# Performance work log

Hardware: AMD Instinct MI355X
Metric: run time of the kernel (lower is better)

The kernel has to match this reference:

```python
import jax, jax.numpy as jnp
import numpy as np
import math

B, N, L = 1, 256, 384
DM, DP, H, D = 256, 128, 8, 32  # d_msa, d_pair, n_head, d_hidden


def ln(x, g, b):
    m = x.mean(-1, keepdims=True)
    v = ((x - m) ** 2).mean(-1, keepdims=True)
    return (x - m) * jax.lax.rsqrt(v + 1e-5) * g + b


def setup_inputs() -> dict:
    key = jax.random.key(0)
    ks = jax.random.split(key, 12)
    s = 0.02
    return dict(
        msa=jax.random.normal(ks[0], (B, N, L, DM), jnp.float32),
        pair=jax.random.normal(ks[1], (B, L, L, DP), jnp.float32),
        ln_msa_g=jnp.ones((DM,), jnp.float32),
        ln_msa_b=jnp.zeros((DM,), jnp.float32),
        ln_pair_g=jnp.ones((DP,), jnp.float32),
        ln_pair_b=jnp.zeros((DP,), jnp.float32),
        sw_wq=s * jax.random.normal(ks[2], (DM, H * D), jnp.float32),
        sw_bq=jnp.zeros((H * D,), jnp.float32),
        sw_wk=s * jax.random.normal(ks[3], (DM, H * D), jnp.float32),
        sw_bk=jnp.zeros((H * D,), jnp.float32),
        wq=s * jax.random.normal(ks[4], (DM, H * D), jnp.float32),
        wk=s * jax.random.normal(ks[5], (DM, H * D), jnp.float32),
        wv=s * jax.random.normal(ks[6], (DM, H * D), jnp.float32),
        wb=s * jax.random.normal(ks[7], (DP, H), jnp.float32),
        wg=s * jax.random.normal(ks[8], (DM, H * D), jnp.float32),
        bg=jnp.ones((H * D,), jnp.float32),
        wo=s * jax.random.normal(ks[9], (H * D, DM), jnp.float32),
        bo=jnp.zeros((DM,), jnp.float32),
    )


def reference(msa, pair, ln_msa_g, ln_msa_b, ln_pair_g, ln_pair_b,
              sw_wq, sw_bq, sw_wk, sw_bk, wq, wk, wv, wb, wg, bg, wo, bo):
    m = ln(msa, ln_msa_g, ln_msa_b)  # (B,N,L,DM) -- LayerNorm(msa)
    inv_sqrt_d = 1.0 / math.sqrt(D)

    # --- SequenceWeight: attention of target seq (row 0) over all MSA rows ---
    qsw = ((m[:, 0] @ sw_wq) + sw_bq).reshape(B, 1, L, H, D) * inv_sqrt_d
    ksw = ((m @ sw_wk) + sw_bk).reshape(B, N, L, H, D)
    sw_logits = jnp.einsum('bqihd,bnihd->bnihq', qsw, ksw)  # (B,N,L,H,1)
    seq_weight = jax.nn.softmax(sw_logits, axis=1)  # softmax over MSA depth N; dropout is eval no-op

    # --- row attention with pair bias ---
    q = (m @ wq).reshape(B, N, L, H, D) * seq_weight  # query scaled by per-row seq weight
    k = (m @ wk).reshape(B, N, L, H, D) * inv_sqrt_d
    attn = jnp.einsum('bnihd,bnjhd->bijh', q, k)  # sum over MSA rows n -> (B,L,L,H)
    attn = attn + ln(pair, ln_pair_g, ln_pair_b) @ wb  # additive pair bias
    attn = jax.nn.softmax(attn, axis=-2)  # softmax over j (dim=-2)

    v = (m @ wv).reshape(B, N, L, H, D)
    out = jnp.einsum('bijh,bnjhd->bnihd', attn, v).reshape(B, N, L, H * D)
    gate = jax.nn.sigmoid((m @ wg) + bg)
    out = out * gate
    return out @ wo + bo  # (B,N,L,DM)
```

## Files before the change

### kernel.cpp

```cpp
#include <hip/hip_runtime.h>
#include <math.h>

typedef unsigned short u16;
typedef __bf16 bf16x8 __attribute__((ext_vector_type(8)));
typedef float f32x4 __attribute__((ext_vector_type(4)));

#define DEV static __device__ __forceinline__

DEV float b2f(u16 u) { union { unsigned int i; float f; } v; v.i = ((unsigned int)u) << 16; return v.f; }
DEV u16 f2b(float f) {
  union { float f; unsigned int i; } v; v.f = f;
  unsigned int x = v.i;
  unsigned int r = (x + 0x7fffu + ((x >> 16) & 1u)) >> 16;
  return (u16)r;
}
DEV bf16x8 load8bf(const u16* p) {
  union { uint4 u; bf16x8 b; } t;
  t.u = *(const uint4*)p;
  return t.b;
}
DEV float wave_sum(float x) {
  for (int m = 32; m >= 1; m >>= 1) x += __shfl_xor(x, m, 64);
  return x;
}
DEV float wave_max(float x) {
  for (int m = 32; m >= 1; m >>= 1) x = fmaxf(x, __shfl_xor(x, m, 64));
  return x;
}

__global__ __launch_bounds__(256) void detect_dtype(const u16* __restrict__ probe, int* __restrict__ flag) {
  __shared__ float red[4];
  int wave = threadIdx.x >> 6, lane = threadIdx.x & 63;
  float v = fabsf(b2f(probe[threadIdx.x]));
  v = wave_max(v);
  if (lane == 0) red[wave] = v;
  __syncthreads();
  if (threadIdx.x == 0) {
    float m = fmaxf(fmaxf(red[0], red[1]), fmaxf(red[2], red[3]));
    *flag = (m > 1e10f) ? 1 : 0;
  }
}

struct SmallCvt {
  const void* src[9];
  int n[9];
  int off[9];
};
__global__ __launch_bounds__(256) void cvt_small(SmallCvt s, u16* __restrict__ dst, const int* __restrict__ flagp) {
  int isf32 = *flagp;
  int a = blockIdx.x;
  const void* sp = s.src[a];
  for (int i = threadIdx.x; i < s.n[a]; i += 256) {
    float v = isf32 ? ((const float*)sp)[i] : b2f(((const u16*)sp)[i]);
    dst[s.off[a] + i] = f2b(v);
  }
}

__global__ __launch_bounds__(256) void ln_msa_k(const void* __restrict__ xv, const u16* __restrict__ g,
                                                const u16* __restrict__ b, u16* __restrict__ out,
                                                const int* __restrict__ flagp) {
  int isf32 = *flagp;
  int wave = threadIdx.x >> 6, lane = threadIdx.x & 63;
  size_t row = (size_t)blockIdx.x * 4 + wave;
  float f0, f1, f2, f3;
  if (isf32) {
    float4 v = *(const float4*)((const float*)xv + row * 256 + lane * 4);
    f0 = v.x; f1 = v.y; f2 = v.z; f3 = v.w;
  } else {
    ushort4 v = *(const ushort4*)((const u16*)xv + row * 256 + lane * 4);
    f0 = b2f(v.x); f1 = b2f(v.y); f2 = b2f(v.z); f3 = b2f(v.w);
  }
  float s = wave_sum(f0 + f1 + f2 + f3);
  float s2 = wave_sum(f0 * f0 + f1 * f1 + f2 * f2 + f3 * f3);
  float mean = s * (1.f / 256.f);
  float inv = rsqrtf(s2 * (1.f / 256.f) - mean * mean + 1e-5f);
  int c0 = lane * 4;
  ushort4 gv = *(const ushort4*)(g + c0);
  ushort4 bv = *(const ushort4*)(b + c0);
  ushort4 o;
  o.x = f2b((f0 - mean) * inv * b2f(gv.x) + b2f(bv.x));
  o.y = f2b((f1 - mean) * inv * b2f(gv.y) + b2f(bv.y));
  o.z = f2b((f2 - mean) * inv * b2f(gv.z) + b2f(bv.z));
  o.w = f2b((f3 - mean) * inv * b2f(gv.w) + b2f(bv.w));
  *(ushort4*)(out + row * 256 + c0) = o;
}

struct TransArgs {
  const void* src[7];
  u16* dst[7];
};
__global__ __launch_bounds__(256) void transpose_w(TransArgs t, const int* __restrict__ flagp) {
  __shared__ float tile[32][33];
  int isf32 = *flagp;
  int m = blockIdx.z;
  const void* s = t.src[m];
  u16* d = t.dst[m];
  int bx = blockIdx.x * 32, by = blockIdx.y * 32;
  int c = threadIdx.x & 31, r0 = threadIdx.x >> 5;
  for (int rr = r0; rr < 32; rr += 8) {
    int idx = (by + rr) * 256 + bx + c;
    tile[rr][c] = isf32 ? ((const float*)s)[idx] : b2f(((const u16*)s)[idx]);
  }
  __syncthreads();
  for (int rr = r0; rr < 32; rr += 8) d[(bx + rr) * 256 + by + c] = f2b(tile[c][rr]);
}

__global__ __launch_bounds__(256) void gemmA(const u16* __restrict__ A, size_t aoff,
                                             const u16* __restrict__ WT, const u16* __restrict__ bias,
                                             void* __restrict__ outv, size_t ooff, int mode, float alpha,
                                             const float* __restrict__ sw, int n0sw,
                                             const int* __restrict__ flagp, int out_flag) {
  int isf32 = *flagp;
  int i0 = blockIdx.x * 128, n0 = blockIdx.y * 128;
  int wave = threadIdx.x >> 6, lane = threadIdx.x & 63;
  int wr = wave >> 1, wc = wave & 1;
  int l15 = lane & 15, quad = lane >> 4;
  const f32x4 fz = {0.f, 0.f, 0.f, 0.f};
  f32x4 acc[4][4];
  for (int mi = 0; mi < 4; ++mi)
    for (int ni = 0; ni < 4; ++ni) acc[mi][ni] = fz;
  int arow = i0 + wr * 64 + l15;
  int brow = n0 + wc * 64 + l15;
  const u16* ap = A + (aoff + (size_t)arow) * 256 + quad * 8;
  const u16* bp = WT + (size_t)brow * 256 + quad * 8;
  for (int k0 = 0; k0 < 256; k0 += 32) {
    bf16x8 a[4], b[4];
#pragma unroll
    for (int mi = 0; mi < 4; ++mi) a[mi] = load8bf(ap + mi * 16 * 256 + k0);
#pragma unroll
    for (int ni = 0; ni < 4; ++ni) b[ni] = load8bf(bp + ni * 16 * 256 + k0);
#pragma unroll
    for (int mi = 0; mi < 4; ++mi)
#pragma unroll
      for (int ni = 0; ni < 4; ++ni)
        acc[mi][ni] = __builtin_amdgcn_mfma_f32_16x16x32_bf16(a[mi], b[ni], acc[mi][ni], 0, 0, 0);
  }
  int f32out = out_flag && isf32;
  int nloc = blockIdx.x / 3;
#pragma unroll
  for (int mi = 0; mi < 4; ++mi) {
    int rbase = i0 + wr * 64 + mi * 16 + quad * 4;
#pragma unroll
    for (int ni = 0; ni < 4; ++ni) {
      int col = n0 + wc * 64 + ni * 16 + l15;
      float bv = bias ? b2f(bias[col]) : 0.f;
#pragma unroll
      for (int r = 0; r < 4; ++r) {
        float val = (acc[mi][ni][r] + bv) * alpha;
        if (mode == 2) {
          int i = rbase - nloc * 384 + r;
          int h = col >> 5;
          val *= sw[((size_t)(i * 8 + h)) * 256 + (n0sw + nloc)];
        }
        size_t idx = (ooff + (size_t)(rbase + r)) * 256 + col;
        if (mode == 1) {
          float gate = 1.f / (1.f + expf(-val));
          ((u16*)outv)[idx] = f2b(b2f(((u16*)outv)[idx]) * gate);
        } else if (f32out) {
          ((float*)outv)[idx] = val;
        } else {
          ((u16*)outv)[idx] = f2b(val);
        }
      }
    }
  }
}

__global__ __launch_bounds__(256) void sw_logits_c(const u16* __restrict__ qsw, const u16* __restrict__ kswc,
                                                   float* __restrict__ swlog, int n0) {
  int nl = blockIdx.y;
  int t = blockIdx.x * 256 + threadIdx.x;
  int i = t >> 3, h = t & 7;
  const u16* kr = kswc + ((size_t)(nl * 384 + i)) * 256 + h * 32;
  const u16* qr = qsw + (size_t)i * 256 + h * 32;
  float dot = 0.f;
#pragma unroll
  for (int d8 = 0; d8 < 4; ++d8) {
    union { uint4 u; u16 us[8]; } ku, qu;
    ku.u = *(const uint4*)(kr + d8 * 8);
    qu.u = *(const uint4*)(qr + d8 * 8);
#pragma unroll
    for (int j = 0; j < 8; ++j) dot += b2f(ku.us[j]) * b2f(qu.us[j]);
  }
  swlog[(size_t)(i * 8 + h) * 256 + n0 + nl] = dot;
}

__global__ __launch_bounds__(256) void sw_softmax(float* __restrict__ swlog) {
  __shared__ float red[4];
  float* p = swlog + (size_t)blockIdx.x * 256;
  int wave = threadIdx.x >> 6, lane = threadIdx.x & 63;
  float x = p[threadIdx.x];
  float m = wave_max(x);
  if (lane == 0) red[wave] = m;
  __syncthreads();
  float mx = fmaxf(fmaxf(red[0], red[1]), fmaxf(red[2], red[3]));
  __syncthreads();
  float e = expf(x - mx);
  float s = wave_sum(e);
  if (lane == 0) red[wave] = s;
  __syncthreads();
  float sum = red[0] + red[1] + red[2] + red[3];
  p[threadIdx.x] = e / sum;
}

__global__ __launch_bounds__(256) void pair_bias(const void* __restrict__ pairv, const u16* __restrict__ g,
                                                 const u16* __restrict__ b, const u16* __restrict__ wb,
                                                 float* __restrict__ attn, const int* __restrict__ flagp) {
  int isf32 = *flagp;
  int wave = threadIdx.x >> 6, lane = threadIdx.x & 63;
  size_t row = (size_t)blockIdx.x * 4 + wave;
  float v0, v1;
  if (isf32) {
    const float* pf = (const float*)pairv + row * 128 + lane * 2;
    v0 = pf[0]; v1 = pf[1];
  } else {
    const u16* pr = (const u16*)pairv + row * 128 + lane * 2;
    v0 = b2f(pr[0]); v1 = b2f(pr[1]);
  }
  float s = wave_sum(v0 + v1);
  float s2 = wave_sum(v0 * v0 + v1 * v1);
  float mean = s * (1.f / 128.f);
  float var = s2 * (1.f / 128.f) - mean * mean;
  float inv = rsqrtf(var + 1e-5f);
  int c0 = lane * 2;
  v0 = (v0 - mean) * inv * b2f(g[c0]) + b2f(b[c0]);
  v1 = (v1 - mean) * inv * b2f(g[c0 + 1]) + b2f(b[c0 + 1]);
  float ph[8];
  const u16* w0 = wb + c0 * 8;
#pragma unroll
  for (int h = 0; h < 8; ++h) ph[h] = v0 * b2f(w0[h]) + v1 * b2f(w0[8 + h]);
#pragma unroll
  for (int m = 32; m >= 1; m >>= 1)
#pragma unroll
    for (int h = 0; h < 8; ++h) ph[h] += __shfl_xor(ph[h], m, 64);
  if (lane == 0) {
#pragma unroll
    for (int h = 0; h < 8; ++h) attn[(size_t)h * 147456 + row] = ph[h];
  }
}

__global__ __launch_bounds__(256) void qk_accum_c(const u16* __restrict__ qc, const u16* __restrict__ kc,
                                                  float* __restrict__ attn, int nlen) {
  int h = blockIdx.y;
  int i0 = (blockIdx.x % 3) * 128, j0 = (blockIdx.x / 3) * 128;
  int nb = blockIdx.z * nlen;
  int wave = threadIdx.x >> 6, lane = threadIdx.x & 63;
  int wr = wave >> 1, wc = wave & 1;
  int l15 = lane & 15, quad = lane >> 4;
  const f32x4 fz = {0.f, 0.f, 0.f, 0.f};
  f32x4 acc[4][4];
  for (int mi = 0; mi < 4; ++mi)
    for (int ni = 0; ni < 4; ++ni) acc[mi][ni] = fz;
  int arow = i0 + wr * 64 + l15;
  int brow = j0 + wc * 64 + l15;
  for (int n = nb; n < nb + nlen; ++n) {
    size_t base = (size_t)n * 384;
    const u16* ap = qc + (base + arow) * 256 + h * 32 + quad * 8;
    const u16* bp = kc + (base + brow) * 256 + h * 32 + quad * 8;
    bf16x8 a[4], b[4];
#pragma unroll
    for (int mi = 0; mi < 4; ++mi) a[mi] = load8bf(ap + mi * 16 * 256);
#pragma unroll
    for (int ni = 0; ni < 4; ++ni) b[ni] = load8bf(bp + ni * 16 * 256);
#pragma unroll
    for (int mi = 0; mi < 4; ++mi)
#pragma unroll
      for (int ni = 0; ni < 4; ++ni)
        acc[mi][ni] = __builtin_amdgcn_mfma_f32_16x16x32_bf16(a[mi], b[ni], acc[mi][ni], 0, 0, 0);
  }
#pragma unroll
  for (int mi = 0; mi < 4; ++mi)
#pragma unroll
    for (int ni = 0; ni < 4; ++ni) {
      int i = i0 + wr * 64 + mi * 16 + quad * 4;
      int j = j0 + wc * 64 + ni * 16 + l15;
#pragma unroll
      for (int r = 0; r < 4; ++r)
        atomicAdd(&attn[(size_t)h * 147456 + (size_t)(i + r) * 384 + j], acc[mi][ni][r]);
    }
}

__global__ __launch_bounds__(384) void attn_softmax_k(const float* __restrict__ attn, u16* __restrict__ attn_bf) {
  __shared__ float red[6];
  size_t r = blockIdx.x;
  const float* p = attn + r * 384;
  int wave = threadIdx.x >> 6, lane = threadIdx.x & 63;
  float x = p[threadIdx.x];
  float m = wave_max(x);
  if (lane == 0) red[wave] = m;
  __syncthreads();
  float mx = red[0];
#pragma unroll
  for (int i = 1; i < 6; ++i) mx = fmaxf(mx, red[i]);
  __syncthreads();
  float e = expf(x - mx);
  float s = wave_sum(e);
  if (lane == 0) red[wave] = s;
  __syncthreads();
  float sum = 0.f;
#pragma unroll
  for (int i = 0; i < 6; ++i) sum += red[i];
  attn_bf[r * 384 + threadIdx.x] = f2b(e / sum);
}

__global__ __launch_bounds__(256) void transpose_v_c(const u16* __restrict__ vc, u16* __restrict__ vt) {
  __shared__ float tile[32][65];
  int nh = blockIdx.y;
  int nl = nh >> 3, h = nh & 7;
  int j0 = blockIdx.x * 64;
  int d = threadIdx.x & 31, jt = threadIdx.x >> 5;
  for (int jj = jt; jj < 64; jj += 8)
    tile[d][jj] = b2f(vc[((size_t)(nl * 384 + j0 + jj)) * 256 + h * 32 + d]);
  __syncthreads();
  int j = threadIdx.x & 63, dq = threadIdx.x >> 6;
  for (int dd = dq; dd < 32; dd += 4)
    vt[((size_t)(nh * 32 + dd)) * 384 + j0 + j] = f2b(tile[dd][j]);
}

__global__ __launch_bounds__(256) void pv_c(const u16* __restrict__ attn_bf, const u16* __restrict__ vt,
                                            u16* __restrict__ oc) {
  int i0 = blockIdx.x * 128;
  int nh = blockIdx.y;
  int nl = nh >> 3, h = nh & 7;
  int w = threadIdx.x >> 6, lane = threadIdx.x & 63;
  int l15 = lane & 15, quad = lane >> 4;
  const f32x4 fz = {0.f, 0.f, 0.f, 0.f};
  f32x4 acc[2][2];
  for (int mi = 0; mi < 2; ++mi)
    for (int ni = 0; ni < 2; ++ni) acc[mi][ni] = fz;
  for (int j0 = 0; j0 < 384; j0 += 32) {
    bf16x8 a[2], b[2];
#pragma unroll
    for (int mi = 0; mi < 2; ++mi)
      a[mi] = load8bf(attn_bf + ((size_t)(h * 384 + i0 + w * 32 + mi * 16 + l15)) * 384 + j0 + quad * 8);
#pragma unroll
    for (int ni = 0; ni < 2; ++ni)
      b[ni] = load8bf(vt + ((size_t)(nh * 32 + ni * 16 + l15)) * 384 + j0 + quad * 8);
#pragma unroll
    for (int mi = 0; mi < 2; ++mi)
#pragma unroll
      for (int ni = 0; ni < 2; ++ni)
        acc[mi][ni] = __builtin_amdgcn_mfma_f32_16x16x32_bf16(a[mi], b[ni], acc[mi][ni], 0, 0, 0);
  }
#pragma unroll
  for (int mi = 0; mi < 2; ++mi)
#pragma unroll
    for (int ni = 0; ni < 2; ++ni) {
      int ib = i0 + w * 32 + mi * 16 + quad * 4;
      int dcol = ni * 16 + l15;
#pragma unroll
      for (int r = 0; r < 4; ++r) {
        size_t idx = ((size_t)(nl * 384 + ib + r)) * 256 + h * 32 + dcol;
        oc[idx] = f2b(acc[mi][ni][r]);
      }
    }
}

extern "C" void kernel_launch(void* const* d_in, const int* in_sizes, int n_in,
                              void* d_out, int out_size, void* d_ws, size_t ws_size,
                              hipStream_t stream) {
  const void* msa = d_in[0];
  const void* pair = d_in[1];
  const void* ln_msa_g = d_in[2];
  const void* ln_msa_b = d_in[3];
  const void* ln_pair_g = d_in[4];
  const void* ln_pair_b = d_in[5];
  const void* sw_wq = d_in[6];
  const void* sw_bq = d_in[7];
  const void* sw_wk = d_in[8];
  const void* sw_bk = d_in[9];
  const void* wq = d_in[10];
  const void* wk = d_in[11];
  const void* wv = d_in[12];
  const void* wb = d_in[13];
  const void* wg = d_in[14];
  const void* bg = d_in[15];
  const void* wo = d_in[16];
  const void* bo = d_in[17];

  char* ws = (char*)d_ws;
  int* flag = (int*)ws;
  float* swlog = (float*)(ws + 256);
  float* attnf = (float*)(ws + 3145984);
  u16* wT = (u16*)(ws + 7864576);
  u16* qswb = (u16*)(ws + 8782080);
  u16* attnbf = (u16*)(ws + 8978688);
  u16* smallv = (u16*)(ws + 11337984);
  u16* mbf = (u16*)(ws + 11343616);
  const size_t SMALLS = 61675264ull;
  u16* c_lng = smallv + 0;
  u16* c_lnb = smallv + 256;
  u16* c_lpg = smallv + 512;
  u16* c_lpb = smallv + 640;
  u16* c_sbq = smallv + 768;
  u16* c_sbk = smallv + 1024;
  u16* c_bg = smallv + 1280;
  u16* c_bo = smallv + 1536;
  u16* c_wb = smallv + 1792;

  int NC = 256;
  while (NC > 8 && SMALLS + 3ull * (size_t)NC * 196608ull > ws_size) NC >>= 1;
  const size_t CBsz = (size_t)NC * 196608ull;
  u16* CB1 = (u16*)(ws + SMALLS);
  u16* CB2 = (u16*)(ws + SMALLS + CBsz);
  u16* CB3 = (u16*)(ws + SMALLS + 2 * CBsz);
  const int nchunks = 256 / NC;
  const int nlen = (NC < 64) ? NC : 64;

  const float isd = 0.17677669529663687f;

  detect_dtype<<<1, 256, 0, stream>>>((const u16*)msa, flag);

  SmallCvt sc;
  sc.src[0] = ln_msa_g;  sc.n[0] = 256;  sc.off[0] = 0;
  sc.src[1] = ln_msa_b;  sc.n[1] = 256;  sc.off[1] = 256;
  sc.src[2] = ln_pair_g; sc.n[2] = 128;  sc.off[2] = 512;
  sc.src[3] = ln_pair_b; sc.n[3] = 128;  sc.off[3] = 640;
  sc.src[4] = sw_bq;     sc.n[4] = 256;  sc.off[4] = 768;
  sc.src[5] = sw_bk;     sc.n[5] = 256;  sc.off[5] = 1024;
  sc.src[6] = bg;        sc.n[6] = 256;  sc.off[6] = 1280;
  sc.src[7] = bo;        sc.n[7] = 256;  sc.off[7] = 1536;
  sc.src[8] = wb;        sc.n[8] = 1024; sc.off[8] = 1792;
  cvt_small<<<9, 256, 0, stream>>>(sc, smallv, flag);

  TransArgs ta;
  ta.src[0] = sw_wq; ta.src[1] = sw_wk; ta.src[2] = wq; ta.src[3] = wk;
  ta.src[4] = wv;    ta.src[5] = wg;    ta.src[6] = wo;
  for (int i = 0; i < 7; ++i) ta.dst[i] = wT + i * 65536;
  transpose_w<<<dim3(8, 8, 7), 256, 0, stream>>>(ta, flag);

  ln_msa_k<<<24576, 256, 0, stream>>>(msa, c_lng, c_lnb, mbf, flag);

  gemmA<<<dim3(3, 2), 256, 0, stream>>>(mbf, 0, wT + 0 * 65536, c_sbq,
                                        qswb, 0, 0, isd, nullptr, 0, flag, 0);

  for (int c = 0; c < nchunks; ++c) {
    size_t R = (size_t)c * NC * 384;
    gemmA<<<dim3(3 * NC, 2), 256, 0, stream>>>(mbf, R, wT + 1 * 65536, c_sbk,
                                               CB1, 0, 0, 1.f, nullptr, 0, flag, 0);
    sw_logits_c<<<dim3(12, NC), 256, 0, stream>>>(qswb, CB1, swlog, c * NC);
  }
  sw_softmax<<<3072, 256, 0, stream>>>(swlog);

  pair_bias<<<36864, 256, 0, stream>>>(pair, c_lpg, c_lpb, c_wb, attnf, flag);
  for (int c = 0; c < nchunks; ++c) {
    size_t R = (size_t)c * NC * 384;
    gemmA<<<dim3(3 * NC, 2), 256, 0, stream>>>(mbf, R, wT + 2 * 65536, nullptr,
                                               CB1, 0, 2, 1.f, swlog, c * NC, flag, 0);
    gemmA<<<dim3(3 * NC, 2), 256, 0, stream>>>(mbf, R, wT + 3 * 65536, nullptr,
                                               CB2, 0, 0, isd, nullptr, 0, flag, 0);
    qk_accum_c<<<dim3(9, 8, NC / nlen), 256, 0, stream>>>(CB1, CB2, attnf, nlen);
  }
  attn_softmax_k<<<3072, 384, 0, stream>>>(attnf, attnbf);

  for (int c = 0; c < nchunks; ++c) {
    size_t R = (size_t)c * NC * 384;
    gemmA<<<dim3(3 * NC, 2), 256, 0, stream>>>(mbf, R, wT + 4 * 65536, nullptr,
                                               CB1, 0, 0, 1.f, nullptr, 0, flag, 0);
    transpose_v_c<<<dim3(6, 8 * NC), 256, 0, stream>>>(CB1, CB2);
    pv_c<<<dim3(3, 8 * NC), 256, 0, stream>>>(attnbf, CB2, CB3);
    gemmA<<<dim3(3 * NC, 2), 256, 0, stream>>>(mbf, R, wT + 5 * 65536, c_bg,
                                               CB3, 0, 1, 1.f, nullptr, 0, flag, 0);
    gemmA<<<dim3(3 * NC, 2), 256, 0, stream>>>(CB3, 0, wT + 6 * 65536, c_bo,
                                               d_out, R, 0, 1.f, nullptr, 0, flag, 1);
  }
}
```

Measured before the change: 1.035 ms.

## Fuse V transpose into projection epilogue and batch PV across MSA rows

The V projection GEMM gains a mode that writes its output already transposed (per row, column-major over sequence positions), so the separate transpose kernel is removed. The PV kernel is rewritten as a larger 128x128-tile GEMM per head that treats (row, d) pairs across four MSA rows as the N dimension, reusing each attention tile across rows. This cuts a kernel launch and a full read/write pass over V and improves MFMA tile utilisation. The cost is strided scalar output stores and an NC divisible-by-4 assumption.

```diff
diff --git a/kernel.cpp b/kernel.cpp
--- a/kernel.cpp
+++ b/kernel.cpp
@@ -137,6 +137,23 @@
   }
   int f32out = out_flag && isf32;
   int nloc = blockIdx.x / 3;
+  if (mode == 3) {
+#pragma unroll
+    for (int mi = 0; mi < 4; ++mi) {
+      int ib = i0 + wr * 64 + mi * 16 + quad * 4 - nloc * 384;
+#pragma unroll
+      for (int ni = 0; ni < 4; ++ni) {
+        int col = n0 + wc * 64 + ni * 16 + l15;
+        ushort4 o;
+        o.x = f2b(acc[mi][ni][0]);
+        o.y = f2b(acc[mi][ni][1]);
+        o.z = f2b(acc[mi][ni][2]);
+        o.w = f2b(acc[mi][ni][3]);
+        *(ushort4*)((u16*)outv + ((size_t)(nloc * 256 + col)) * 384 + ib) = o;
+      }
+    }
+    return;
+  }
 #pragma unroll
   for (int mi = 0; mi < 4; ++mi) {
     int rbase = i0 + wr * 64 + mi * 16 + quad * 4;
@@ -303,57 +320,50 @@
   attn_bf[r * 384 + threadIdx.x] = f2b(e / sum);
 }
 
-__global__ __launch_bounds__(256) void transpose_v_c(const u16* __restrict__ vc, u16* __restrict__ vt) {
-  __shared__ float tile[32][65];
-  int nh = blockIdx.y;
-  int nl = nh >> 3, h = nh & 7;
-  int j0 = blockIdx.x * 64;
-  int d = threadIdx.x & 31, jt = threadIdx.x >> 5;
-  for (int jj = jt; jj < 64; jj += 8)
-    tile[d][jj] = b2f(vc[((size_t)(nl * 384 + j0 + jj)) * 256 + h * 32 + d]);
-  __syncthreads();
-  int j = threadIdx.x & 63, dq = threadIdx.x >> 6;
-  for (int dd = dq; dd < 32; dd += 4)
-    vt[((size_t)(nh * 32 + dd)) * 384 + j0 + j] = f2b(tile[dd][j]);
-}
-
-__global__ __launch_bounds__(256) void pv_c(const u16* __restrict__ attn_bf, const u16* __restrict__ vt,
-                                            u16* __restrict__ oc) {
+__global__ __launch_bounds__(256) void pv_gemm(const u16* __restrict__ attn_bf, const u16* __restrict__ vt,
+                                               u16* __restrict__ oc) {
+  int h = blockIdx.z;
   int i0 = blockIdx.x * 128;
-  int nh = blockIdx.y;
-  int nl = nh >> 3, h = nh & 7;
-  int w = threadIdx.x >> 6, lane = threadIdx.x & 63;
+  int c0 = blockIdx.y * 128;
+  int wave = threadIdx.x >> 6, lane = threadIdx.x & 63;
+  int wr = wave >> 1, wc = wave & 1;
   int l15 = lane & 15, quad = lane >> 4;
   const f32x4 fz = {0.f, 0.f, 0.f, 0.f};
-  f32x4 acc[2][2];
-  for (int mi = 0; mi < 2; ++mi)
-    for (int ni = 0; ni < 2; ++ni) acc[mi][ni] = fz;
-  for (int j0 = 0; j0 < 384; j0 += 32) {
-    bf16x8 a[2], b[2];
-#pragma unroll
-    for (int mi = 0; mi < 2; ++mi)
-      a[mi] = load8bf(attn_bf + ((size_t)(h * 384 + i0 + w * 32 + mi * 16 + l15)) * 384 + j0 + quad * 8);
-#pragma unroll
-    for (int ni = 0; ni < 2; ++ni)
-      b[ni] = load8bf(vt + ((size_t)(nh * 32 + ni * 16 + l15)) * 384 + j0 + quad * 8);
-#pragma unroll
-    for (int mi = 0; mi < 2; ++mi)
-#pragma unroll
-      for (int ni = 0; ni < 2; ++ni)
+  f32x4 acc[4][4];
+  for (int mi = 0; mi < 4; ++mi)
+    for (int ni = 0; ni < 4; ++ni) acc[mi][ni] = fz;
+  int arow = i0 + wr * 64 + l15;
+  const u16* ap = attn_bf + ((size_t)(h * 384 + arow)) * 384 + quad * 8;
+  const u16* bp[4];
+#pragma unroll
+  for (int ni = 0; ni < 4; ++ni) {
+    int col = c0 + wc * 64 + ni * 16 + l15;
+    bp[ni] = vt + ((size_t)((col >> 5) * 256 + h * 32 + (col & 31))) * 384 + quad * 8;
+  }
+  for (int k0 = 0; k0 < 384; k0 += 32) {
+    bf16x8 a[4], b[4];
+#pragma unroll
+    for (int mi = 0; mi < 4; ++mi) a[mi] = load8bf(ap + mi * 16 * 384 + k0);
+#pragma unroll
+    for (int ni = 0; ni < 4; ++ni) b[ni] = load8bf(bp[ni] + k0);
+#pragma unroll
+    for (int mi = 0; mi < 4; ++mi)
+#pragma unroll
+      for (int ni = 0; ni < 4; ++ni)
         acc[mi][ni] = __builtin_amdgcn_mfma_f32_16x16x32_bf16(a[mi], b[ni], acc[mi][ni], 0, 0, 0);
   }
 #pragma unroll
-  for (int mi = 0; mi < 2; ++mi)
-#pragma unroll
-    for (int ni = 0; ni < 2; ++ni) {
-      int ib = i0 + w * 32 + mi * 16 + quad * 4;
-      int dcol = ni * 16 + l15;
-#pragma unroll
-      for (int r = 0; r < 4; ++r) {
-        size_t idx = ((size_t)(nl * 384 + ib + r)) * 256 + h * 32 + dcol;
-        oc[idx] = f2b(acc[mi][ni][r]);
-      }
+  for (int mi = 0; mi < 4; ++mi) {
+    int ib = i0 + wr * 64 + mi * 16 + quad * 4;
+#pragma unroll
+    for (int ni = 0; ni < 4; ++ni) {
+      int col = c0 + wc * 64 + ni * 16 + l15;
+      int nl = col >> 5, d = col & 31;
+#pragma unroll
+      for (int r = 0; r < 4; ++r)
+        oc[((size_t)(nl * 384 + ib + r)) * 256 + h * 32 + d] = f2b(acc[mi][ni][r]);
     }
+  }
 }
 
 extern "C" void kernel_launch(void* const* d_in, const int* in_sizes, int n_in,
@@ -456,9 +466,8 @@
   for (int c = 0; c < nchunks; ++c) {
     size_t R = (size_t)c * NC * 384;
     gemmA<<<dim3(3 * NC, 2), 256, 0, stream>>>(mbf, R, wT + 4 * 65536, nullptr,
-                                               CB1, 0, 0, 1.f, nullptr, 0, flag, 0);
-    transpose_v_c<<<dim3(6, 8 * NC), 256, 0, stream>>>(CB1, CB2);
-    pv_c<<<dim3(3, 8 * NC), 256, 0, stream>>>(attnbf, CB2, CB3);
+                                               CB2, 0, 3, 1.f, nullptr, 0, flag, 0);
+    pv_gemm<<<dim3(3, NC / 4, 8), 256, 0, stream>>>(attnbf, CB2, CB3);
     gemmA<<<dim3(3 * NC, 2), 256, 0, stream>>>(mbf, R, wT + 5 * 65536, c_bg,
                                                CB3, 0, 1, 1.f, nullptr, 0, flag, 0);
     gemmA<<<dim3(3 * NC, 2), 256, 0, stream>>>(CB3, 0, wT + 6 * 65536, c_bo,
```

After: 1.009 ms. 1.03x faster.
